# Kernel tuning notes

Measured on AMD Instinct MI355X. Metric: run time of the kernel, lower is better.

Reference implementation:

```python
import jax, jax.numpy as jnp
import numpy as np

WORLD_SIZE = 1
EXPERT_NUM = 8
D_MODEL = 1024
D_HIDDEN = 4096
TOK_PER_EXPERT = 2048


def setup_inputs() -> dict:
    key = jax.random.key(0)
    k1, k2, k3 = jax.random.split(key, 3)
    x = jax.random.normal(k1, (EXPERT_NUM, TOK_PER_EXPERT, D_MODEL), dtype=jnp.float32)
    # kaiming_uniform-like scale for faithfulness of magnitudes
    bound1 = 1.0 / np.sqrt(D_MODEL)
    bound2 = 1.0 / np.sqrt(D_HIDDEN)
    weight1 = jax.random.uniform(k2, (EXPERT_NUM, D_HIDDEN, D_MODEL), dtype=jnp.float32, minval=-bound1, maxval=bound1)
    weight2 = jax.random.uniform(k3, (EXPERT_NUM, D_MODEL, D_HIDDEN), dtype=jnp.float32, minval=-bound2, maxval=bound2)
    return {"x": x, "weight1": weight1, "weight2": weight2}


def reference(x, weight1, weight2):
    # x -> (world_size, expert_num, tokens, d_model)
    xr = x.reshape(WORLD_SIZE, EXPERT_NUM, -1, D_MODEL)
    # grouped GEMM 1 + ReLU: [g,e,s,m] x [e,h,m] -> [g,e,s,h]
    ffn1 = jax.nn.relu(jnp.einsum('gesm,ehm->gesh', xr, weight1))
    # grouped GEMM 2: [g,e,s,h] x [e,m,h] -> [g,e,s,m]
    y = jnp.einsum('gesh,emh->gesm', ffn1, weight2)
    return y
```

## Files before the change

### kernel.cpp

```cpp
#include <hip/hip_runtime.h>
#include <hip/hip_bf16.h>

#define EXPERTS 8
#define TOK 2048
#define DM 1024
#define DH 4096

#define BM 128
#define BN 128
#define BK 32
#define LSTR 40

typedef __bf16 bf16x8 __attribute__((ext_vector_type(8)));
typedef float  f32x4  __attribute__((ext_vector_type(4)));

static __device__ __forceinline__ bf16x8 cvt8(float4 a, float4 b) {
    bf16x8 r;
    r[0] = (__bf16)a.x; r[1] = (__bf16)a.y; r[2] = (__bf16)a.z; r[3] = (__bf16)a.w;
    r[4] = (__bf16)b.x; r[5] = (__bf16)b.y; r[6] = (__bf16)b.z; r[7] = (__bf16)b.w;
    return r;
}

static __device__ __forceinline__ void gload16(const __bf16* g, __bf16* l) {
    __builtin_amdgcn_global_load_lds(
        (__attribute__((address_space(1))) void*)g,
        (__attribute__((address_space(3))) void*)l, 16, 0, 0);
}

#define BARRIER() asm volatile("s_barrier" ::: "memory")
#define LGKMC(n)  do { asm volatile("s_waitcnt lgkmcnt(" #n ")" ::: "memory"); \
                       __builtin_amdgcn_sched_barrier(0); } while (0)
#define VMW8()    asm volatile("s_waitcnt vmcnt(8)" ::: "memory")
#define VMW0()    asm volatile("s_waitcnt vmcnt(0)" ::: "memory")

__global__ __launch_bounds__(256)
void cvt_all(const float* __restrict__ x,  const float* __restrict__ w1,
             const float* __restrict__ w2, __bf16* __restrict__ xb,
             __bf16* __restrict__ w1b,     __bf16* __restrict__ w2b,
             int nx, int nw1, int ntot) {
    int i = blockIdx.x * blockDim.x + threadIdx.x;
    const int stride = gridDim.x * blockDim.x;
    for (; i < ntot; i += stride) {
        const float* src; __bf16* dst; int off;
        if (i < nx)            { src = x;  dst = xb;  off = i; }
        else if (i < nx + nw1) { src = w1; dst = w1b; off = i - nx; }
        else                   { src = w2; dst = w2b; off = i - nx - nw1; }
        const float4* p = (const float4*)src + (size_t)off * 2;
        float4 a = p[0], b = p[1];
        *((bf16x8*)dst + off) = cvt8(a, b);
    }
}

template<bool RELU, bool OUT_BF16>
__global__ __launch_bounds__(512, 2)
void gemm8(const __bf16* __restrict__ Ap, const __bf16* __restrict__ Bp,
           void* __restrict__ Cp, int N, int K, int tiles_m, int tiles_n,
           size_t sA, size_t sB, size_t sC)
{
    __shared__ __bf16 lds[2][2][16384];

    int bid = blockIdx.x;
    const int chunk = gridDim.x >> 3;
    bid = (bid & 7) * chunk + (bid >> 3);

    const int per_e = tiles_m * tiles_n;
    const int e  = bid / per_e;
    const int tt = bid - e * per_e;
    const int tn = tt / tiles_m;
    const int tm = tt - tn * tiles_m;

    const int tid = threadIdx.x;
    const int l   = tid & 63;
    const int wid = tid >> 6;
    const int wr  = wid >> 2;
    const int wc  = wid & 3;
    const int lr  = l & 15;
    const int kg  = l >> 4;
    const int lq  = l >> 3;
    const int swz_e = ((l & 7) ^ lq) << 3;

    const int cc0  = (kg * 16) ^ ((l & 7) << 4);
    const int cc1  = cc0 ^ 64;
    const int rowA = (wr * 128 + lr) * 128;
    const int rowB = (wc * 64  + lr) * 128;

    const __bf16* Ag = Ap + e * sA + (size_t)(tm * 256) * K;
    const __bf16* Bg = Bp + e * sB + (size_t)(tn * 256) * K;

    auto stage_half = [&](const __bf16* g, int mat, int c2, int h, int kt2) {
        const __bf16* s0 = g + (size_t)(h * 128 + wid * 8 + lq) * K + kt2 * 64 + swz_e;
        gload16(s0,                  &lds[c2][mat][h * 8192 + wid * 512]);
        gload16(s0 + (size_t)64 * K, &lds[c2][mat][h * 8192 + 4096 + wid * 512]);
    };

    f32x4 acc[8][4];
    #pragma unroll
    for (int m = 0; m < 8; ++m)
        #pragma unroll
        for (int n = 0; n < 4; ++n)
            acc[m][n] = (f32x4){0.f, 0.f, 0.f, 0.f};

    const int NT = K / 64;

    stage_half(Ag, 0, 0, 0, 0); stage_half(Ag, 0, 0, 1, 0);
    stage_half(Bg, 1, 0, 0, 0); stage_half(Bg, 1, 0, 1, 0);
    stage_half(Ag, 0, 1, 0, 1); stage_half(Ag, 0, 1, 1, 1);
    stage_half(Bg, 1, 1, 0, 1); stage_half(Bg, 1, 1, 1, 1);
    VMW8();
    BARRIER();

    bf16x8 a[4][2], a2[4][2], b0[2][2], b1[2][2];
    {
        const char* Ab = (const char*)&lds[0][0][0] + rowA;
        const char* Bb = (const char*)&lds[0][1][0] + rowB;
        #pragma unroll
        for (int mf = 0; mf < 4; ++mf) {
            a[mf][0] = *(const bf16x8*)(Ab + mf * 2048 + cc0);
            a[mf][1] = *(const bf16x8*)(Ab + mf * 2048 + cc1);
        }
        #pragma unroll
        for (int nf = 0; nf < 2; ++nf) {
            b0[nf][0] = *(const bf16x8*)(Bb + nf * 2048 + cc0);
            b0[nf][1] = *(const bf16x8*)(Bb + nf * 2048 + cc1);
        }
    }

    for (int t = 0; t < NT; ++t) {
        const int c = t & 1;
        const char* Ab  = (const char*)&lds[c][0][0] + rowA;
        const char* Bb  = (const char*)&lds[c][1][0] + rowB;
        const char* Abn = (const char*)&lds[c ^ 1][0][0] + rowA;
        const char* Bbn = (const char*)&lds[c ^ 1][1][0] + rowB;
        const bool pf   = (t + 2 < NT);
        const bool more = (t + 1 < NT);

        #pragma unroll
        for (int nf = 0; nf < 2; ++nf) {
            b1[nf][0] = *(const bf16x8*)(Bb + (2 + nf) * 2048 + cc0);
            b1[nf][1] = *(const bf16x8*)(Bb + (2 + nf) * 2048 + cc1);
        }
        LGKMC(4);
        BARRIER();
        __builtin_amdgcn_s_setprio(1);
        #pragma unroll
        for (int mf = 0; mf < 4; ++mf)
            #pragma unroll
            for (int nf = 0; nf < 2; ++nf) {
                acc[mf][nf] = __builtin_amdgcn_mfma_f32_16x16x32_bf16(a[mf][0], b0[nf][0], acc[mf][nf], 0, 0, 0);
                acc[mf][nf] = __builtin_amdgcn_mfma_f32_16x16x32_bf16(a[mf][1], b0[nf][1], acc[mf][nf], 0, 0, 0);
            }
        __builtin_amdgcn_s_setprio(0);

        #pragma unroll
        for (int mf = 0; mf < 4; ++mf) {
            a2[mf][0] = *(const bf16x8*)(Ab + (4 + mf) * 2048 + cc0);
            a2[mf][1] = *(const bf16x8*)(Ab + (4 + mf) * 2048 + cc1);
        }
        LGKMC(8);
        BARRIER();
        if (pf) { stage_half(Bg, 1, c, 0, t + 2); stage_half(Bg, 1, c, 1, t + 2); }
        __builtin_amdgcn_s_setprio(1);
        #pragma unroll
        for (int mf = 0; mf < 4; ++mf)
            #pragma unroll
            for (int nf = 0; nf < 2; ++nf) {
                acc[mf][2 + nf] = __builtin_amdgcn_mfma_f32_16x16x32_bf16(a[mf][0], b1[nf][0], acc[mf][2 + nf], 0, 0, 0);
                acc[mf][2 + nf] = __builtin_amdgcn_mfma_f32_16x16x32_bf16(a[mf][1], b1[nf][1], acc[mf][2 + nf], 0, 0, 0);
            }
        __builtin_amdgcn_s_setprio(0);

        LGKMC(0);
        BARRIER();
        if (pf) { stage_half(Ag, 0, c, 0, t + 2); stage_half(Ag, 0, c, 1, t + 2); }
        __builtin_amdgcn_s_setprio(1);
        #pragma unroll
        for (int mf = 0; mf < 4; ++mf)
            #pragma unroll
            for (int nf = 0; nf < 2; ++nf) {
                acc[4 + mf][2 + nf] = __builtin_amdgcn_mfma_f32_16x16x32_bf16(a2[mf][0], b1[nf][0], acc[4 + mf][2 + nf], 0, 0, 0);
                acc[4 + mf][2 + nf] = __builtin_amdgcn_mfma_f32_16x16x32_bf16(a2[mf][1], b1[nf][1], acc[4 + mf][2 + nf], 0, 0, 0);
            }
        __builtin_amdgcn_s_setprio(0);

        if (more) { if (pf) VMW8(); else VMW0(); }
        BARRIER();
        if (more) {
            #pragma unroll
            for (int mf = 0; mf < 4; ++mf) {
                a[mf][0] = *(const bf16x8*)(Abn + mf * 2048 + cc0);
                a[mf][1] = *(const bf16x8*)(Abn + mf * 2048 + cc1);
            }
        }
        __builtin_amdgcn_s_setprio(1);
        #pragma unroll
        for (int mf = 0; mf < 4; ++mf)
            #pragma unroll
            for (int nf = 0; nf < 2; ++nf) {
                acc[4 + mf][nf] = __builtin_amdgcn_mfma_f32_16x16x32_bf16(a2[mf][0], b0[nf][0], acc[4 + mf][nf], 0, 0, 0);
                acc[4 + mf][nf] = __builtin_amdgcn_mfma_f32_16x16x32_bf16(a2[mf][1], b0[nf][1], acc[4 + mf][nf], 0, 0, 0);
            }
        __builtin_amdgcn_s_setprio(0);
        if (more) {
            #pragma unroll
            for (int nf = 0; nf < 2; ++nf) {
                b0[nf][0] = *(const bf16x8*)(Bbn + nf * 2048 + cc0);
                b0[nf][1] = *(const bf16x8*)(Bbn + nf * 2048 + cc1);
            }
        }
    }

    const int orow = tm * 256 + wr * 128 + kg * 4;
    const int ocol = tn * 256 + wc * 64 + lr;
    if constexpr (OUT_BF16) {
        __bf16* C = (__bf16*)Cp + e * sC;
        #pragma unroll
        for (int mf = 0; mf < 8; ++mf)
            #pragma unroll
            for (int j = 0; j < 4; ++j) {
                const size_t base = (size_t)(orow + mf * 16 + j) * N + ocol;
                #pragma unroll
                for (int nf = 0; nf < 4; ++nf) {
                    float v = acc[mf][nf][j];
                    if (RELU) v = fmaxf(v, 0.f);
                    C[base + nf * 16] = (__bf16)v;
                }
            }
    } else {
        float* C = (float*)Cp + e * sC;
        #pragma unroll
        for (int mf = 0; mf < 8; ++mf)
            #pragma unroll
            for (int j = 0; j < 4; ++j) {
                const size_t base = (size_t)(orow + mf * 16 + j) * N + ocol;
                #pragma unroll
                for (int nf = 0; nf < 4; ++nf) {
                    float v = acc[mf][nf][j];
                    if (RELU) v = fmaxf(v, 0.f);
                    C[base + nf * 16] = v;
                }
            }
    }
}

template<int AMODE, int BMODE, bool RELU, bool OUT_BF16>
__global__ __launch_bounds__(256)
void gemm2(const void* __restrict__ Ap, const void* __restrict__ Bp,
           void* __restrict__ Cp, int N, int K, int tiles_m, int tiles_n,
           size_t sA, size_t sB, size_t sC)
{
    constexpr int LA = (AMODE == 0) ? BK : LSTR;
    constexpr int LB = (BMODE == 0) ? BK : LSTR;
    __shared__ __bf16 As[BM * LA];
    __shared__ __bf16 Bs[BN * LB];

    int bid = blockIdx.x;
    const int chunk = gridDim.x >> 3;
    bid = (bid & 7) * chunk + (bid >> 3);

    const int per_e = tiles_m * tiles_n;
    const int e  = bid / per_e;
    const int t  = bid - e * per_e;
    const int tn = t / tiles_m;
    const int tm = t - tn * tiles_m;

    const int tid = threadIdx.x;
    const int l   = tid & 63;
    const int wid = tid >> 6;
    const int wr  = wid >> 1, wc = wid & 1;
    const int lr  = l & 15;
    const int kg  = l >> 4;
    const int srow = tid >> 1;
    const int scol = (tid & 1) << 4;

    const __bf16* gA = nullptr; __bf16* lA = nullptr;
    const float*  pAf = nullptr; __bf16* aWr = nullptr;
    float4 A0, A1, A2, A3;
    if constexpr (AMODE == 0) {
        gA = (const __bf16*)Ap + e * sA
           + (size_t)(tm * BM + wid * 16 + (l >> 2)) * K + (l & 3) * 8;
        lA = As + wid * 512;
    } else {
        pAf = (const float*)Ap + e * sA + (size_t)(tm * BM + srow) * K + scol;
        aWr = As + srow * LA + scol;
        A0 = *(const float4*)(pAf);      A1 = *(const float4*)(pAf + 4);
        A2 = *(const float4*)(pAf + 8);  A3 = *(const float4*)(pAf + 12);
    }
    const __bf16* gB = nullptr; __bf16* lB = nullptr;
    const float*  pBf = nullptr; __bf16* bWr = nullptr;
    float4 B0, B1, B2, B3;
    if constexpr (BMODE == 0) {
        gB = (const __bf16*)Bp + e * sB
           + (size_t)(tn * BN + wid * 16 + (l >> 2)) * K + (l & 3) * 8;
        lB = Bs + wid * 512;
    } else {
        pBf = (const float*)Bp + e * sB + (size_t)(tn * BN + srow) * K + scol;
        bWr = Bs + srow * LB + scol;
        B0 = *(const float4*)(pBf);      B1 = *(const float4*)(pBf + 4);
        B2 = *(const float4*)(pBf + 8);  B3 = *(const float4*)(pBf + 12);
    }

    const __bf16* aRd = As + (wr * 64 + lr) * LA + kg * 8;
    const __bf16* bRd = Bs + (wc * 64 + lr) * LB + kg * 8;

    f32x4 acc[4][4];
    #pragma unroll
    for (int m = 0; m < 4; ++m)
        #pragma unroll
        for (int n = 0; n < 4; ++n)
            acc[m][n] = (f32x4){0.f, 0.f, 0.f, 0.f};

    const int NT = K / BK;
    for (int kt = 0; kt < NT; ++kt) {
        if (kt) __syncthreads();
        if constexpr (AMODE == 0) {
            gload16(gA, lA);
            gload16(gA + (size_t)64 * K, lA + 2048);
            gA += BK;
        } else {
            *(bf16x8*)(aWr)     = cvt8(A0, A1);
            *(bf16x8*)(aWr + 8) = cvt8(A2, A3);
        }
        if constexpr (BMODE == 0) {
            gload16(gB, lB);
            gload16(gB + (size_t)64 * K, lB + 2048);
            gB += BK;
        } else {
            *(bf16x8*)(bWr)     = cvt8(B0, B1);
            *(bf16x8*)(bWr + 8) = cvt8(B2, B3);
        }
        __syncthreads();

        if (kt + 1 < NT) {
            if constexpr (AMODE == 2) {
                pAf += BK;
                A0 = *(const float4*)(pAf);      A1 = *(const float4*)(pAf + 4);
                A2 = *(const float4*)(pAf + 8);  A3 = *(const float4*)(pAf + 12);
            }
            if constexpr (BMODE == 2) {
                pBf += BK;
                B0 = *(const float4*)(pBf);      B1 = *(const float4*)(pBf + 4);
                B2 = *(const float4*)(pBf + 8);  B3 = *(const float4*)(pBf + 12);
            }
        }

        bf16x8 af[4], bfr[4];
        #pragma unroll
        for (int m = 0; m < 4; ++m) af[m]  = *(const bf16x8*)(aRd + m * 16 * LA);
        #pragma unroll
        for (int n = 0; n < 4; ++n) bfr[n] = *(const bf16x8*)(bRd + n * 16 * LB);
        #pragma unroll
        for (int m = 0; m < 4; ++m)
            #pragma unroll
            for (int n = 0; n < 4; ++n)
                acc[m][n] = __builtin_amdgcn_mfma_f32_16x16x32_bf16(af[m], bfr[n], acc[m][n], 0, 0, 0);
    }

    const int orow = tm * BM + wr * 64 + kg * 4;
    const int ocol = tn * BN + wc * 64 + lr;
    if constexpr (OUT_BF16) {
        __bf16* C = (__bf16*)Cp + e * sC;
        #pragma unroll
        for (int m = 0; m < 4; ++m)
            #pragma unroll
            for (int j = 0; j < 4; ++j) {
                const size_t base = (size_t)(orow + m * 16 + j) * N + ocol;
                #pragma unroll
                for (int n = 0; n < 4; ++n) {
                    float v = acc[m][n][j];
                    if (RELU) v = fmaxf(v, 0.f);
                    C[base + n * 16] = (__bf16)v;
                }
            }
    } else {
        float* C = (float*)Cp + e * sC;
        #pragma unroll
        for (int m = 0; m < 4; ++m)
            #pragma unroll
            for (int j = 0; j < 4; ++j) {
                const size_t base = (size_t)(orow + m * 16 + j) * N + ocol;
                #pragma unroll
                for (int n = 0; n < 4; ++n) {
                    float v = acc[m][n][j];
                    if (RELU) v = fmaxf(v, 0.f);
                    C[base + n * 16] = v;
                }
            }
    }
}

extern "C" void kernel_launch(void* const* d_in, const int* in_sizes, int n_in,
                              void* d_out, int out_size, void* d_ws, size_t ws_size,
                              hipStream_t stream) {
    const float* x  = (const float*)d_in[0];
    const float* w1 = (const float*)d_in[1];
    const float* w2 = (const float*)d_in[2];
    float* out = (float*)d_out;

    const size_t SZ_F  = (size_t)EXPERTS * TOK * DH * sizeof(__bf16);
    const size_t SZ_X  = (size_t)EXPERTS * TOK * DM * sizeof(__bf16);
    const size_t SZ_W1 = (size_t)EXPERTS * DH * DM * sizeof(__bf16);
    const size_t SZ_W2 = (size_t)EXPERTS * DM * DH * sizeof(__bf16);

    char* wsb = (char*)d_ws;
    __bf16* ffn1 = (__bf16*)wsb;

    const dim3 blk(256);
    const dim3 cgrid(2048);
    const int NX  = EXPERTS * TOK * DM / 8;
    const int NW1 = EXPERTS * DH * DM / 8;
    const int NW2 = EXPERTS * DM * DH / 8;

    const size_t eA1 = (size_t)TOK * DM, eB1 = (size_t)DH * DM, eC1 = (size_t)TOK * DH;
    const size_t eA2 = (size_t)TOK * DH, eB2 = (size_t)DM * DH, eC2 = (size_t)TOK * DM;

    if (ws_size >= SZ_F + SZ_X + SZ_W1 + SZ_W2) {
        __bf16* xb  = (__bf16*)(wsb + SZ_F);
        __bf16* w1b = (__bf16*)(wsb + SZ_F + SZ_X);
        __bf16* w2b = (__bf16*)(wsb + SZ_F + SZ_X + SZ_W1);
        hipLaunchKernelGGL(cvt_all, cgrid, blk, 0, stream,
            x, w1, w2, xb, w1b, w2b, NX, NW1, NX + NW1 + NW2);
        const dim3 g1(EXPERTS * (TOK / 256) * (DH / 256));
        const dim3 g2(EXPERTS * (TOK / 256) * (DM / 256));
        hipLaunchKernelGGL((gemm8<true, true>), g1, dim3(512), 0, stream,
            xb, w1b, ffn1, DH, DM, TOK / 256, DH / 256, eA1, eB1, eC1);
        hipLaunchKernelGGL((gemm8<false, false>), g2, dim3(512), 0, stream,
            ffn1, w2b, out, DM, DH, TOK / 256, DM / 256, eA2, eB2, eC2);
    } else if (ws_size >= SZ_F + SZ_X + SZ_W1) {
        __bf16* xb  = (__bf16*)(wsb + SZ_F);
        __bf16* w1b = (__bf16*)(wsb + SZ_F + SZ_X);
        hipLaunchKernelGGL(cvt_all, cgrid, blk, 0, stream,
            x, w1, w1, xb, w1b, w1b, NX, NW1, NX + NW1);
        const dim3 g1(EXPERTS * (TOK / 256) * (DH / 256));
        const dim3 g2(EXPERTS * (TOK / BM) * (DM / BN));
        hipLaunchKernelGGL((gemm8<true, true>), g1, dim3(512), 0, stream,
            xb, w1b, ffn1, DH, DM, TOK / 256, DH / 256, eA1, eB1, eC1);
        hipLaunchKernelGGL((gemm2<0, 2, false, false>), g2, blk, 0, stream,
            ffn1, w2, out, DM, DH, TOK / BM, DM / BN, eA2, eB2, eC2);
    } else if (ws_size >= SZ_F + SZ_W1) {
        __bf16* w1b = (__bf16*)(wsb + SZ_F);
        hipLaunchKernelGGL(cvt_all, cgrid, blk, 0, stream,
            w1, w1, w1, w1b, w1b, w1b, NW1, 0, NW1);
        const dim3 g1(EXPERTS * (TOK / BM) * (DH / BN));
        const dim3 g2(EXPERTS * (TOK / BM) * (DM / BN));
        hipLaunchKernelGGL((gemm2<2, 0, true, true>), g1, blk, 0, stream,
            x, w1b, ffn1, DH, DM, TOK / BM, DH / BN, eA1, eB1, eC1);
        hipLaunchKernelGGL((gemm2<0, 2, false, false>), g2, blk, 0, stream,
            ffn1, w2, out, DM, DH, TOK / BM, DM / BN, eA2, eB2, eC2);
    } else if (ws_size >= SZ_F) {
        const dim3 g1(EXPERTS * (TOK / BM) * (DH / BN));
        const dim3 g2(EXPERTS * (TOK / BM) * (DM / BN));
        hipLaunchKernelGGL((gemm2<2, 2, true, true>), g1, blk, 0, stream,
            x, w1, ffn1, DH, DM, TOK / BM, DH / BN, eA1, eB1, eC1);
        hipLaunchKernelGGL((gemm2<0, 2, false, false>), g2, blk, 0, stream,
            ffn1, w2, out, DM, DH, TOK / BM, DM / BN, eA2, eB2, eC2);
    } else {
        int rows = (int)((ws_size / ((size_t)DH * sizeof(__bf16))) / BM) * BM;
        if (rows <= 0) rows = BM;
        if (rows > TOK) rows = TOK;
        for (int e = 0; e < EXPERTS; ++e) {
            for (int r0 = 0; r0 < TOK; r0 += rows) {
                int mr = (TOK - r0 < rows) ? (TOK - r0) : rows;
                dim3 cg1((mr / BM) * (DH / BN));
                hipLaunchKernelGGL((gemm2<2, 2, true, true>), cg1, blk, 0, stream,
                    x + ((size_t)e * TOK + r0) * DM, w1 + (size_t)e * DH * DM, ffn1,
                    DH, DM, mr / BM, DH / BN, (size_t)0, (size_t)0, (size_t)0);
                dim3 cg2((mr / BM) * (DM / BN));
                hipLaunchKernelGGL((gemm2<0, 2, false, false>), cg2, blk, 0, stream,
                    ffn1, w2 + (size_t)e * DM * DH, out + ((size_t)e * TOK + r0) * DM,
                    DM, DH, mr / BM, DM / BN, (size_t)0, (size_t)0, (size_t)0);
            }
        }
    }
}
```

Measured before the change: 364.5 us.

## Restructure GEMM main loop into 8-phase ping-pong schedule with interleaved staging

Replaces the per-K-tile loop with a two-tile unrolled loop split into eight phases. Each phase issues its LDS fragment reads and one half-tile global-to-LDS load, then synchronises with barriers before a block of MFMAs. Global loads are spread evenly across phases with a tighter vmcnt(4) wait, and the A tile for the next buffer is staged later instead of in the prologue. The aim is finer-grained overlap of memory and MFMA work across the two waves sharing a SIMD. The cost is more barriers and full lgkmcnt(0) drains per phase, and the buffer reuse timing now depends on delicate ordering.

```diff
diff --git a/kernel.cpp b/kernel.cpp
--- a/kernel.cpp
+++ b/kernel.cpp
@@ -28,9 +28,10 @@
 }
 
 #define BARRIER() asm volatile("s_barrier" ::: "memory")
-#define LGKMC(n)  do { asm volatile("s_waitcnt lgkmcnt(" #n ")" ::: "memory"); \
+#define LGKM0()   do { asm volatile("s_waitcnt lgkmcnt(0)" ::: "memory"); \
                        __builtin_amdgcn_sched_barrier(0); } while (0)
-#define VMW8()    asm volatile("s_waitcnt vmcnt(8)" ::: "memory")
+#define LGKM8()   asm volatile("s_waitcnt lgkmcnt(8)" ::: "memory")
+#define VMW4()    asm volatile("s_waitcnt vmcnt(4)" ::: "memory")
 #define VMW0()    asm volatile("s_waitcnt vmcnt(0)" ::: "memory")
 
 __global__ __launch_bounds__(256)
@@ -100,113 +101,103 @@
         for (int n = 0; n < 4; ++n)
             acc[m][n] = (f32x4){0.f, 0.f, 0.f, 0.f};
 
+    const char* A0b = (const char*)&lds[0][0][0] + rowA;
+    const char* B0b = (const char*)&lds[0][1][0] + rowB;
+    const char* A1b = (const char*)&lds[1][0][0] + rowA;
+    const char* B1b = (const char*)&lds[1][1][0] + rowB;
+
+    bf16x8 al[4][2], ah[4][2], bl[2][2], bh[2][2];
+
+    auto rdA = [&](bf16x8 (&dst)[4][2], const char* base, int half) {
+        #pragma unroll
+        for (int mf = 0; mf < 4; ++mf) {
+            dst[mf][0] = *(const bf16x8*)(base + (half * 4 + mf) * 2048 + cc0);
+            dst[mf][1] = *(const bf16x8*)(base + (half * 4 + mf) * 2048 + cc1);
+        }
+    };
+    auto rdB = [&](bf16x8 (&dst)[2][2], const char* base, int half) {
+        #pragma unroll
+        for (int nf = 0; nf < 2; ++nf) {
+            dst[nf][0] = *(const bf16x8*)(base + (half * 2 + nf) * 2048 + cc0);
+            dst[nf][1] = *(const bf16x8*)(base + (half * 2 + nf) * 2048 + cc1);
+        }
+    };
+    auto mma16 = [&](bf16x8 (&af)[4][2], bf16x8 (&bf_)[2][2], int mo, int no) {
+        __builtin_amdgcn_s_setprio(1);
+        #pragma unroll
+        for (int mf = 0; mf < 4; ++mf)
+            #pragma unroll
+            for (int nf = 0; nf < 2; ++nf) {
+                acc[mo + mf][no + nf] = __builtin_amdgcn_mfma_f32_16x16x32_bf16(af[mf][0], bf_[nf][0], acc[mo + mf][no + nf], 0, 0, 0);
+                acc[mo + mf][no + nf] = __builtin_amdgcn_mfma_f32_16x16x32_bf16(af[mf][1], bf_[nf][1], acc[mo + mf][no + nf], 0, 0, 0);
+            }
+        __builtin_amdgcn_s_setprio(0);
+    };
+
     const int NT = K / 64;
+    const int NI = NT / 2;
 
     stage_half(Ag, 0, 0, 0, 0); stage_half(Ag, 0, 0, 1, 0);
     stage_half(Bg, 1, 0, 0, 0); stage_half(Bg, 1, 0, 1, 0);
-    stage_half(Ag, 0, 1, 0, 1); stage_half(Ag, 0, 1, 1, 1);
     stage_half(Bg, 1, 1, 0, 1); stage_half(Bg, 1, 1, 1, 1);
-    VMW8();
+    VMW4();
     BARRIER();
 
-    bf16x8 a[4][2], a2[4][2], b0[2][2], b1[2][2];
-    {
-        const char* Ab = (const char*)&lds[0][0][0] + rowA;
-        const char* Bb = (const char*)&lds[0][1][0] + rowB;
-        #pragma unroll
-        for (int mf = 0; mf < 4; ++mf) {
-            a[mf][0] = *(const bf16x8*)(Ab + mf * 2048 + cc0);
-            a[mf][1] = *(const bf16x8*)(Ab + mf * 2048 + cc1);
-        }
-        #pragma unroll
-        for (int nf = 0; nf < 2; ++nf) {
-            b0[nf][0] = *(const bf16x8*)(Bb + nf * 2048 + cc0);
-            b0[nf][1] = *(const bf16x8*)(Bb + nf * 2048 + cc1);
-        }
-    }
-
-    for (int t = 0; t < NT; ++t) {
-        const int c = t & 1;
-        const char* Ab  = (const char*)&lds[c][0][0] + rowA;
-        const char* Bb  = (const char*)&lds[c][1][0] + rowB;
-        const char* Abn = (const char*)&lds[c ^ 1][0][0] + rowA;
-        const char* Bbn = (const char*)&lds[c ^ 1][1][0] + rowB;
-        const bool pf   = (t + 2 < NT);
-        const bool more = (t + 1 < NT);
-
-        #pragma unroll
-        for (int nf = 0; nf < 2; ++nf) {
-            b1[nf][0] = *(const bf16x8*)(Bb + (2 + nf) * 2048 + cc0);
-            b1[nf][1] = *(const bf16x8*)(Bb + (2 + nf) * 2048 + cc1);
-        }
-        LGKMC(4);
-        BARRIER();
-        __builtin_amdgcn_s_setprio(1);
-        #pragma unroll
-        for (int mf = 0; mf < 4; ++mf)
-            #pragma unroll
-            for (int nf = 0; nf < 2; ++nf) {
-                acc[mf][nf] = __builtin_amdgcn_mfma_f32_16x16x32_bf16(a[mf][0], b0[nf][0], acc[mf][nf], 0, 0, 0);
-                acc[mf][nf] = __builtin_amdgcn_mfma_f32_16x16x32_bf16(a[mf][1], b0[nf][1], acc[mf][nf], 0, 0, 0);
-            }
-        __builtin_amdgcn_s_setprio(0);
-
-        #pragma unroll
-        for (int mf = 0; mf < 4; ++mf) {
-            a2[mf][0] = *(const bf16x8*)(Ab + (4 + mf) * 2048 + cc0);
-            a2[mf][1] = *(const bf16x8*)(Ab + (4 + mf) * 2048 + cc1);
-        }
-        LGKMC(8);
-        BARRIER();
-        if (pf) { stage_half(Bg, 1, c, 0, t + 2); stage_half(Bg, 1, c, 1, t + 2); }
-        __builtin_amdgcn_s_setprio(1);
-        #pragma unroll
-        for (int mf = 0; mf < 4; ++mf)
-            #pragma unroll
-            for (int nf = 0; nf < 2; ++nf) {
-                acc[mf][2 + nf] = __builtin_amdgcn_mfma_f32_16x16x32_bf16(a[mf][0], b1[nf][0], acc[mf][2 + nf], 0, 0, 0);
-                acc[mf][2 + nf] = __builtin_amdgcn_mfma_f32_16x16x32_bf16(a[mf][1], b1[nf][1], acc[mf][2 + nf], 0, 0, 0);
-            }
-        __builtin_amdgcn_s_setprio(0);
-
-        LGKMC(0);
-        BARRIER();
-        if (pf) { stage_half(Ag, 0, c, 0, t + 2); stage_half(Ag, 0, c, 1, t + 2); }
-        __builtin_amdgcn_s_setprio(1);
-        #pragma unroll
-        for (int mf = 0; mf < 4; ++mf)
-            #pragma unroll
-            for (int nf = 0; nf < 2; ++nf) {
-                acc[4 + mf][2 + nf] = __builtin_amdgcn_mfma_f32_16x16x32_bf16(a2[mf][0], b1[nf][0], acc[4 + mf][2 + nf], 0, 0, 0);
-                acc[4 + mf][2 + nf] = __builtin_amdgcn_mfma_f32_16x16x32_bf16(a2[mf][1], b1[nf][1], acc[4 + mf][2 + nf], 0, 0, 0);
-            }
-        __builtin_amdgcn_s_setprio(0);
-
-        if (more) { if (pf) VMW8(); else VMW0(); }
-        BARRIER();
-        if (more) {
-            #pragma unroll
-            for (int mf = 0; mf < 4; ++mf) {
-                a[mf][0] = *(const bf16x8*)(Abn + mf * 2048 + cc0);
-                a[mf][1] = *(const bf16x8*)(Abn + mf * 2048 + cc1);
-            }
-        }
-        __builtin_amdgcn_s_setprio(1);
-        #pragma unroll
-        for (int mf = 0; mf < 4; ++mf)
-            #pragma unroll
-            for (int nf = 0; nf < 2; ++nf) {
-                acc[4 + mf][nf] = __builtin_amdgcn_mfma_f32_16x16x32_bf16(a2[mf][0], b0[nf][0], acc[4 + mf][nf], 0, 0, 0);
-                acc[4 + mf][nf] = __builtin_amdgcn_mfma_f32_16x16x32_bf16(a2[mf][1], b0[nf][1], acc[4 + mf][nf], 0, 0, 0);
-            }
-        __builtin_amdgcn_s_setprio(0);
-        if (more) {
-            #pragma unroll
-            for (int nf = 0; nf < 2; ++nf) {
-                b0[nf][0] = *(const bf16x8*)(Bbn + nf * 2048 + cc0);
-                b0[nf][1] = *(const bf16x8*)(Bbn + nf * 2048 + cc1);
-            }
-        }
+    for (int it = 0; it < NI; ++it) {
+        const int To = 2 * it + 1;
+        const int Te = 2 * it + 2;
+        const int Tn = 2 * it + 3;
+        const bool pf = (it + 1 < NI);
+
+        rdA(al, A0b, 0); rdB(bl, B0b, 0);
+        stage_half(Ag, 0, 1, 0, To);
+        LGKM8();
+        BARRIER(); LGKM0();
+        mma16(al, bl, 0, 0);
+        BARRIER();
+
+        rdB(bh, B0b, 1);
+        stage_half(Ag, 0, 1, 1, To);
+        BARRIER(); LGKM0();
+        mma16(al, bh, 0, 2);
+        BARRIER();
+
+        rdA(ah, A0b, 1);
+        if (pf) stage_half(Bg, 1, 0, 0, Te);
+        BARRIER(); LGKM0();
+        mma16(ah, bh, 4, 2);
+        BARRIER();
+
+        if (pf) stage_half(Bg, 1, 0, 1, Te);
+        BARRIER();
+        mma16(ah, bl, 4, 0);
+        if (pf) VMW4(); else VMW0();
+        BARRIER();
+
+        rdA(al, A1b, 0); rdB(bl, B1b, 0);
+        if (pf) stage_half(Ag, 0, 0, 0, Te);
+        LGKM8();
+        BARRIER(); LGKM0();
+        mma16(al, bl, 0, 0);
+        BARRIER();
+
+        rdB(bh, B1b, 1);
+        if (pf) stage_half(Ag, 0, 0, 1, Te);
+        BARRIER(); LGKM0();
+        mma16(al, bh, 0, 2);
+        BARRIER();
+
+        rdA(ah, A1b, 1);
+        if (pf) stage_half(Bg, 1, 1, 0, Tn);
+        BARRIER(); LGKM0();
+        mma16(ah, bh, 4, 2);
+        BARRIER();
+
+        if (pf) stage_half(Bg, 1, 1, 1, Tn);
+        BARRIER();
+        mma16(ah, bl, 4, 0);
+        if (pf) VMW4();
+        BARRIER();
     }
 
     const int orow = tm * 256 + wr * 128 + kg * 4;
```

Measured after the change: 349.5 us. 1.04x faster.
